# Optimization experiments

Measured on AMD Instinct MI355X. Metric: run time of the kernel, lower is better.

The kernel has to match this reference:

```python
import jax, jax.numpy as jnp
import numpy as np

EMBED_DIM = 1024
ATTN_DIM = 1024
BATCH = 4
SEQ = 2048


def setup_inputs() -> dict:
    key = jax.random.key(0)
    k1, k2, k3, k4 = jax.random.split(key, 4)
    embedded = jax.random.normal(k1, (BATCH, SEQ, EMBED_DIM), dtype=jnp.float32)
    # torch Linear weights have shape [out_features, in_features]
    scale = 1.0 / np.sqrt(EMBED_DIM)
    W_K = jax.random.uniform(k2, (ATTN_DIM, EMBED_DIM), dtype=jnp.float32, minval=-scale, maxval=scale)
    W_Q = jax.random.uniform(k3, (ATTN_DIM, EMBED_DIM), dtype=jnp.float32, minval=-scale, maxval=scale)
    W_V = jax.random.uniform(k4, (ATTN_DIM, EMBED_DIM), dtype=jnp.float32, minval=-scale, maxval=scale)
    return {"embedded": embedded, "W_K": W_K, "W_Q": W_Q, "W_V": W_V}


def reference(embedded, W_K, W_Q, W_V):
    # embedded: [B, L, E]; W_*: [A, E] (torch Linear layout, applied as x @ W.T)
    L = embedded.shape[1]
    A = W_K.shape[0]
    K = jnp.einsum('ble,ae->bla', embedded, W_K)
    Q = jnp.einsum('ble,ae->bla', embedded, W_Q)
    V = jnp.einsum('ble,ae->bla', embedded, W_V)
    att = jnp.einsum('bqa,bka->bqk', Q, K) / jnp.sqrt(jnp.float32(A))  # [B, L, L]
    causal = jnp.tril(jnp.ones((L, L), dtype=bool))  # lower-triangular mask
    att = jnp.where(causal, att, -jnp.inf)
    att = jax.nn.softmax(att, axis=-1)
    return jnp.einsum('bqk,bka->bqa', att, V)
```

## Files before the change

### kernel.cpp

```cpp
#include <hip/hip_runtime.h>
#include <hip/hip_bf16.h>
#include <stdint.h>

#define BATCH 4
#define SEQ   2048
#define EMB   1024
#define ADIM  1024

typedef __attribute__((ext_vector_type(8))) short  short8;
typedef __attribute__((ext_vector_type(4))) float  float4v;

static __device__ __forceinline__ unsigned short f2bf(float f) {
    unsigned int u = __float_as_uint(f);
    u += 0x7FFFu + ((u >> 16) & 1u);
    return (unsigned short)(u >> 16);
}

static __device__ __forceinline__ uint2 pack4(float4v v) {
    uint2 r;
    r.x = (unsigned)f2bf(v.x) | ((unsigned)f2bf(v.y) << 16);
    r.y = (unsigned)f2bf(v.z) | ((unsigned)f2bf(v.w) << 16);
    return r;
}

static __device__ __forceinline__ void gload16(const void* g, void* l) {
    __builtin_amdgcn_global_load_lds(
        (const __attribute__((address_space(1))) void*)g,
        (__attribute__((address_space(3))) void*)l, 16, 0, 0);
}

__global__ __launch_bounds__(256) void zero_kernel(float* __restrict__ p)
{
    const int i = (blockIdx.x * 256 + threadIdx.x) * 4;
    *(float4v*)(p + i) = float4v{0.f, 0.f, 0.f, 0.f};
}

__global__ __launch_bounds__(256) void cvt_all_kernel(
    const float* __restrict__ X,  const float* __restrict__ Wk,
    const float* __restrict__ Wq, const float* __restrict__ Wv,
    unsigned short* __restrict__ Xb,  unsigned short* __restrict__ Wkb,
    unsigned short* __restrict__ Wqb, unsigned short* __restrict__ Wvb)
{
    const int bI = blockIdx.x;
    const float* src; unsigned short* dst; int off;
    if (bI < 4096)      { src = X;  dst = Xb;  off = bI; }
    else if (bI < 4608) { src = Wk; dst = Wkb; off = bI - 4096; }
    else if (bI < 5120) { src = Wq; dst = Wqb; off = bI - 4608; }
    else                { src = Wv; dst = Wvb; off = bI - 5120; }
    const int i = (off * 256 + threadIdx.x) * 8;
    float4v a = *(const float4v*)(src + i);
    float4v b = *(const float4v*)(src + i + 4);
    uint2 pa = pack4(a), pb = pack4(b);
    uint4 o; o.x = pa.x; o.y = pa.y; o.z = pb.x; o.w = pb.y;
    *(uint4*)(dst + i) = o;
}

static __device__ __forceinline__ void gemm_core(
    const unsigned short* __restrict__ A, const unsigned short* __restrict__ B,
    int lda, int ldb, int m0, int n0, int kend,
    unsigned short* As, unsigned short* Bs, float4v acc[4][4])
{
    const int tid  = threadIdx.x;
    const int r    = tid >> 2;
    const int c8   = (tid & 3) << 3;
    const int lane = tid & 63;
    const int wave = tid >> 6;
    const int quad = lane >> 4;
    const int l16  = lane & 15;
    const int wm   = (wave >> 1) << 6;
    const int wn   = (wave & 1) << 6;

    const unsigned short* Ag = A + (size_t)(m0 + r) * lda + c8;
    const unsigned short* Bg = B + (size_t)(n0 + r) * ldb + c8;
    unsigned short* Al = As + tid * 8;
    unsigned short* Bl = Bs + tid * 8;
    const int niter = kend >> 5;

    #define ISSUE(k0, st) do { \
        unsigned short* al_ = Al + (st) * 4096; \
        unsigned short* bl_ = Bl + (st) * 4096; \
        gload16(Ag + (k0),                        al_); \
        gload16(Ag + (k0) + (size_t)64 * lda,     al_ + 2048); \
        gload16(Bg + (k0),                        bl_); \
        gload16(Bg + (k0) + (size_t)64 * ldb,     bl_ + 2048); \
    } while (0)

    ISSUE(0, 0);
    ISSUE(32, 1);

    int ci = 0;
    int ii = 2;
    for (int it = 0; it < niter; ++it) {
        const int knext = (it + 2 < niter) ? ((it + 2) << 5) : 0;
        ISSUE(knext, ii);
        asm volatile("s_waitcnt vmcnt(8)" ::: "memory");
        asm volatile("s_barrier" ::: "memory");

        const unsigned short* Ah = As + ci * 4096;
        const unsigned short* Bh = Bs + ci * 4096;
        short8 af[4], bfr[4];
        #pragma unroll
        for (int i = 0; i < 4; ++i)
            af[i] = *(const short8*)&Ah[(wm + 16 * i + l16) * 32 + quad * 8];
        #pragma unroll
        for (int j = 0; j < 4; ++j)
            bfr[j] = *(const short8*)&Bh[(wn + 16 * j + l16) * 32 + quad * 8];
        #pragma unroll
        for (int i = 0; i < 4; ++i)
            #pragma unroll
            for (int j = 0; j < 4; ++j)
                acc[i][j] = __builtin_amdgcn_mfma_f32_16x16x32_bf16(af[i], bfr[j], acc[i][j], 0, 0, 0);

        asm volatile("s_barrier" ::: "memory");
        ci = (ci == 2) ? 0 : ci + 1;
        ii = (ii == 2) ? 0 : ii + 1;
    }
    asm volatile("s_waitcnt vmcnt(0)" ::: "memory");
    #undef ISSUE
}

#define DECL_TILE_IDX() \
    const int lane = threadIdx.x & 63; \
    const int wave = threadIdx.x >> 6; \
    const int quad = lane >> 4; \
    const int l16  = lane & 15; \
    const int wm   = (wave >> 1) << 6; \
    const int wn   = (wave & 1) << 6;

__global__ __launch_bounds__(256, 3) void qkv_kernel(
    const unsigned short* __restrict__ Xb, const unsigned short* __restrict__ Wqb,
    const unsigned short* __restrict__ Wkb, const unsigned short* __restrict__ Wvb,
    unsigned short* __restrict__ Qb, unsigned short* __restrict__ Kb,
    unsigned short* __restrict__ Vtb)
{
    __shared__ __align__(16) unsigned short As[3 * 128 * 32];
    __shared__ __align__(16) unsigned short Bs[3 * 128 * 32];
    const int idx   = blockIdx.x;
    const int mlow  = idx & 7;
    const int n0    = ((idx >> 3) & 7) << 7;
    const int rest  = idx >> 6;
    const int mhigh = rest & 7;
    const int z     = rest >> 3;
    const int m0    = ((mhigh << 3) | mlow) << 7;
    const unsigned short* W = (z == 0) ? Wqb : (z == 1) ? Wkb : Wvb;

    float4v acc[4][4];
    #pragma unroll
    for (int i = 0; i < 4; ++i)
        #pragma unroll
        for (int j = 0; j < 4; ++j)
            acc[i][j] = float4v{0.f, 0.f, 0.f, 0.f};

    gemm_core(Xb, W, EMB, EMB, m0, n0, EMB, As, Bs, acc);

    DECL_TILE_IDX();
    #pragma unroll
    for (int i = 0; i < 4; ++i)
        #pragma unroll
        for (int j = 0; j < 4; ++j)
            #pragma unroll
            for (int rr = 0; rr < 4; ++rr) {
                const int row = m0 + wm + 16 * i + quad * 4 + rr;
                const int col = n0 + wn + 16 * j + l16;
                const unsigned short v = f2bf(acc[i][j][rr]);
                if (z == 0)      Qb[(size_t)row * ADIM + col] = v;
                else if (z == 1) Kb[(size_t)row * ADIM + col] = v;
                else {
                    const int bb = row >> 11;
                    const int l  = row & (SEQ - 1);
                    Vtb[((size_t)(bb * ADIM + col) << 11) + l] = v;
                }
            }
}

__global__ __launch_bounds__(256, 3) void s_kernel(
    const unsigned short* __restrict__ Qb, const unsigned short* __restrict__ Kb,
    unsigned short* __restrict__ E, float* __restrict__ rowsum)
{
    const int idx = blockIdx.x;
    const int b   = idx & 3;
    const int tri = idx >> 2;
    int qt = 0;
    while (((qt + 1) * (qt + 2)) / 2 <= tri) ++qt;
    const int kt = tri - (qt * (qt + 1)) / 2;
    const int q0 = qt << 7;
    const int k0 = kt << 7;

    __shared__ __align__(16) unsigned short As[3 * 128 * 32];
    __shared__ __align__(16) unsigned short Bs[3 * 128 * 32];

    float4v acc[4][4];
    #pragma unroll
    for (int i = 0; i < 4; ++i)
        #pragma unroll
        for (int j = 0; j < 4; ++j)
            acc[i][j] = float4v{0.f, 0.f, 0.f, 0.f};

    gemm_core(Qb + (size_t)b * SEQ * ADIM, Kb + (size_t)b * SEQ * ADIM,
              ADIM, ADIM, q0, k0, ADIM, As, Bs, acc);

    unsigned short* Eb = E + (size_t)b * SEQ * SEQ;
    float* rsb = rowsum + (size_t)b * SEQ;
    DECL_TILE_IDX();
    const float scale = 0.03125f;
    #pragma unroll
    for (int i = 0; i < 4; ++i)
        #pragma unroll
        for (int rr = 0; rr < 4; ++rr) {
            const int row = q0 + wm + 16 * i + quad * 4 + rr;
            float s = 0.f;
            #pragma unroll
            for (int j = 0; j < 4; ++j) {
                const int col = k0 + wn + 16 * j + l16;
                float e = (col <= row) ? __expf(acc[i][j][rr] * scale) : 0.f;
                s += e;
                Eb[(size_t)row * SEQ + col] = f2bf(e);
            }
            s += __shfl_xor(s, 1);
            s += __shfl_xor(s, 2);
            s += __shfl_xor(s, 4);
            s += __shfl_xor(s, 8);
            if (l16 == 0) atomicAdd(&rsb[row], s);
        }
}

__global__ __launch_bounds__(256, 3) void pv_kernel(
    const unsigned short* __restrict__ E, const unsigned short* __restrict__ Vtb,
    const float* __restrict__ rowsum, float* __restrict__ out)
{
    const int idx = blockIdx.x;
    const int t   = 15 - (idx >> 5);
    const int rem = idx & 31;
    const int b   = rem >> 3;
    const int a0  = (rem & 7) << 7;
    const int q0  = t << 7;

    __shared__ __align__(16) unsigned short As[3 * 128 * 32];
    __shared__ __align__(16) unsigned short Bs[3 * 128 * 32];

    float4v acc[4][4];
    #pragma unroll
    for (int i = 0; i < 4; ++i)
        #pragma unroll
        for (int j = 0; j < 4; ++j)
            acc[i][j] = float4v{0.f, 0.f, 0.f, 0.f};

    gemm_core(E + (size_t)b * SEQ * SEQ, Vtb + (size_t)b * ADIM * SEQ,
              SEQ, SEQ, q0, a0, q0 + 128, As, Bs, acc);

    float* ob = out + (size_t)b * SEQ * ADIM;
    const float* rsb = rowsum + (size_t)b * SEQ;
    DECL_TILE_IDX();
    #pragma unroll
    for (int i = 0; i < 4; ++i)
        #pragma unroll
        for (int rr = 0; rr < 4; ++rr) {
            const int row = q0 + wm + 16 * i + quad * 4 + rr;
            const float inv = 1.0f / rsb[row];
            #pragma unroll
            for (int j = 0; j < 4; ++j) {
                const int col = a0 + wn + 16 * j + l16;
                ob[(size_t)row * ADIM + col] = acc[i][j][rr] * inv;
            }
        }
}

extern "C" void kernel_launch(void* const* d_in, const int* in_sizes, int n_in,
                              void* d_out, int out_size, void* d_ws, size_t ws_size,
                              hipStream_t stream)
{
    const float* X  = (const float*)d_in[0];
    const float* Wk = (const float*)d_in[1];
    const float* Wq = (const float*)d_in[2];
    const float* Wv = (const float*)d_in[3];
    float* out = (float*)d_out;

    const size_t MB = 1024 * 1024;
    char* ws = (char*)d_ws;
    unsigned short* Xb  = (unsigned short*)(ws);
    unsigned short* Wqb = (unsigned short*)(ws + 16 * MB);
    unsigned short* Wkb = (unsigned short*)(ws + 18 * MB);
    unsigned short* Wvb = (unsigned short*)(ws + 20 * MB);
    unsigned short* E   = (unsigned short*)(ws);
    unsigned short* Qb  = (unsigned short*)(ws + 64 * MB);
    unsigned short* Kb  = (unsigned short*)(ws + 80 * MB);
    unsigned short* Vtb = (unsigned short*)(ws + 96 * MB);
    float*          rowsum = (float*)(ws + 112 * MB);

    hipLaunchKernelGGL(zero_kernel, dim3(BATCH * SEQ / 1024), dim3(256), 0, stream, rowsum);
    hipLaunchKernelGGL(cvt_all_kernel, dim3(5632), dim3(256), 0, stream,
                       X, Wk, Wq, Wv, Xb, Wkb, Wqb, Wvb);
    hipLaunchKernelGGL(qkv_kernel, dim3(1536), dim3(256), 0, stream,
                       Xb, Wqb, Wkb, Wvb, Qb, Kb, Vtb);
    hipLaunchKernelGGL(s_kernel, dim3(4 * 136), dim3(256), 0, stream, Qb, Kb, E, rowsum);
    hipLaunchKernelGGL(pv_kernel, dim3(512), dim3(256), 0, stream, E, Vtb, rowsum, out);
}
```

Before: 252.0 us.

## Fold W_Q and W_K into a single matrix to drop the K projection

Precomputes M = W_Q^T W_K (scaled) as a weight-only GEMM, then forms Q' = X·M and uses X directly as keys in the score GEMM, so the separate K projection GEMM is removed. A transposing bf16 conversion kernel is added for W_Q and W_K, and the rowsum zeroing is merged into the conversion kernel, cutting one launch. The cost is an extra small 1024x1024x1024 GEMM, and precision shifts because M is rounded to bf16 before it is applied.

Result: no change. 256.8 us (+1.9%).

```diff
diff --git a/kernel.cpp b/kernel.cpp
--- a/kernel.cpp
+++ b/kernel.cpp
@@ -29,30 +29,57 @@
         (__attribute__((address_space(3))) void*)l, 16, 0, 0);
 }
 
-__global__ __launch_bounds__(256) void zero_kernel(float* __restrict__ p)
-{
-    const int i = (blockIdx.x * 256 + threadIdx.x) * 4;
-    *(float4v*)(p + i) = float4v{0.f, 0.f, 0.f, 0.f};
-}
-
 __global__ __launch_bounds__(256) void cvt_all_kernel(
-    const float* __restrict__ X,  const float* __restrict__ Wk,
-    const float* __restrict__ Wq, const float* __restrict__ Wv,
-    unsigned short* __restrict__ Xb,  unsigned short* __restrict__ Wkb,
-    unsigned short* __restrict__ Wqb, unsigned short* __restrict__ Wvb)
+    const float* __restrict__ X,  const float* __restrict__ Wv,
+    unsigned short* __restrict__ Xb, unsigned short* __restrict__ Wvb,
+    float* __restrict__ rowsum)
 {
     const int bI = blockIdx.x;
+    if (bI >= 4608) {
+        const int i = ((bI - 4608) * 256 + threadIdx.x) * 4;
+        *(float4v*)(rowsum + i) = float4v{0.f, 0.f, 0.f, 0.f};
+        return;
+    }
     const float* src; unsigned short* dst; int off;
-    if (bI < 4096)      { src = X;  dst = Xb;  off = bI; }
-    else if (bI < 4608) { src = Wk; dst = Wkb; off = bI - 4096; }
-    else if (bI < 5120) { src = Wq; dst = Wqb; off = bI - 4608; }
-    else                { src = Wv; dst = Wvb; off = bI - 5120; }
+    if (bI < 4096) { src = X;  dst = Xb;  off = bI; }
+    else           { src = Wv; dst = Wvb; off = bI - 4096; }
     const int i = (off * 256 + threadIdx.x) * 8;
     float4v a = *(const float4v*)(src + i);
     float4v b = *(const float4v*)(src + i + 4);
     uint2 pa = pack4(a), pb = pack4(b);
     uint4 o; o.x = pa.x; o.y = pa.y; o.z = pb.x; o.w = pb.y;
     *(uint4*)(dst + i) = o;
+}
+
+__global__ __launch_bounds__(256) void tcvt_kernel(
+    const float* __restrict__ Wq, const float* __restrict__ Wk,
+    unsigned short* __restrict__ WqT, unsigned short* __restrict__ WkT)
+{
+    __shared__ unsigned short T[64][72];
+    const int z    = blockIdx.x >> 8;
+    const int tile = blockIdx.x & 255;
+    const int ti = tile >> 4;
+    const int tj = tile & 15;
+    const float* W = z ? Wk : Wq;
+    unsigned short* WT = z ? WkT : WqT;
+    const int t  = threadIdx.x;
+    const int r  = t >> 2;
+    const int c  = (t & 3) << 4;
+
+    const float* src = W + (size_t)(ti * 64 + r) * EMB + tj * 64 + c;
+    #pragma unroll
+    for (int u = 0; u < 4; ++u) {
+        float4v v = *(const float4v*)(src + 4 * u);
+        uint2 p = pack4(v);
+        *(uint2*)&T[r][c + 4 * u] = p;
+    }
+    __syncthreads();
+    unsigned short tmp[16];
+    #pragma unroll
+    for (int u = 0; u < 16; ++u) tmp[u] = T[c + u][r];
+    unsigned short* dst = WT + (size_t)(tj * 64 + r) * EMB + ti * 64 + c;
+    *(uint4*)(dst)     = *(uint4*)&tmp[0];
+    *(uint4*)(dst + 8) = *(uint4*)&tmp[8];
 }
 
 static __device__ __forceinline__ void gemm_core(
@@ -79,17 +106,16 @@
     #define ISSUE(k0, st) do { \
         unsigned short* al_ = Al + (st) * 4096; \
         unsigned short* bl_ = Bl + (st) * 4096; \
-        gload16(Ag + (k0),                        al_); \
-        gload16(Ag + (k0) + (size_t)64 * lda,     al_ + 2048); \
-        gload16(Bg + (k0),                        bl_); \
-        gload16(Bg + (k0) + (size_t)64 * ldb,     bl_ + 2048); \
+        gload16(Ag + (k0),                    al_); \
+        gload16(Ag + (k0) + (size_t)64 * lda, al_ + 2048); \
+        gload16(Bg + (k0),                    bl_); \
+        gload16(Bg + (k0) + (size_t)64 * ldb, bl_ + 2048); \
     } while (0)
 
     ISSUE(0, 0);
     ISSUE(32, 1);
 
-    int ci = 0;
-    int ii = 2;
+    int ci = 0, ii = 2;
     for (int it = 0; it < niter; ++it) {
         const int knext = (it + 2 < niter) ? ((it + 2) << 5) : 0;
         ISSUE(knext, ii);
@@ -127,22 +153,52 @@
     const int wm   = (wave >> 1) << 6; \
     const int wn   = (wave & 1) << 6;
 
-__global__ __launch_bounds__(256, 3) void qkv_kernel(
-    const unsigned short* __restrict__ Xb, const unsigned short* __restrict__ Wqb,
-    const unsigned short* __restrict__ Wkb, const unsigned short* __restrict__ Wvb,
-    unsigned short* __restrict__ Qb, unsigned short* __restrict__ Kb,
-    unsigned short* __restrict__ Vtb)
+__global__ __launch_bounds__(256, 3) void m_kernel(
+    const unsigned short* __restrict__ WkT, const unsigned short* __restrict__ WqT,
+    unsigned short* __restrict__ Mt)
+{
+    __shared__ __align__(16) unsigned short As[3 * 128 * 32];
+    __shared__ __align__(16) unsigned short Bs[3 * 128 * 32];
+    const int m0 = (blockIdx.x >> 3) << 7;
+    const int n0 = (blockIdx.x & 7) << 7;
+
+    float4v acc[4][4];
+    #pragma unroll
+    for (int i = 0; i < 4; ++i)
+        #pragma unroll
+        for (int j = 0; j < 4; ++j)
+            acc[i][j] = float4v{0.f, 0.f, 0.f, 0.f};
+
+    gemm_core(WkT, WqT, EMB, EMB, m0, n0, EMB, As, Bs, acc);
+
+    DECL_TILE_IDX();
+    const float scale = 0.03125f;
+    #pragma unroll
+    for (int i = 0; i < 4; ++i)
+        #pragma unroll
+        for (int j = 0; j < 4; ++j)
+            #pragma unroll
+            for (int rr = 0; rr < 4; ++rr) {
+                const int row = m0 + wm + 16 * i + quad * 4 + rr;
+                const int col = n0 + wn + 16 * j + l16;
+                Mt[(size_t)row * EMB + col] = f2bf(acc[i][j][rr] * scale);
+            }
+}
+
+__global__ __launch_bounds__(256, 3) void qv_kernel(
+    const unsigned short* __restrict__ Xb, const unsigned short* __restrict__ Mt,
+    const unsigned short* __restrict__ Wvb,
+    unsigned short* __restrict__ Qpb, unsigned short* __restrict__ Vtb)
 {
     __shared__ __align__(16) unsigned short As[3 * 128 * 32];
     __shared__ __align__(16) unsigned short Bs[3 * 128 * 32];
     const int idx   = blockIdx.x;
     const int mlow  = idx & 7;
     const int n0    = ((idx >> 3) & 7) << 7;
-    const int rest  = idx >> 6;
-    const int mhigh = rest & 7;
-    const int z     = rest >> 3;
+    const int mhigh = (idx >> 6) & 7;
+    const int z     = idx >> 9;
     const int m0    = ((mhigh << 3) | mlow) << 7;
-    const unsigned short* W = (z == 0) ? Wqb : (z == 1) ? Wkb : Wvb;
+    const unsigned short* W = (z == 0) ? Mt : Wvb;
 
     float4v acc[4][4];
     #pragma unroll
@@ -163,8 +219,7 @@
                 const int row = m0 + wm + 16 * i + quad * 4 + rr;
                 const int col = n0 + wn + 16 * j + l16;
                 const unsigned short v = f2bf(acc[i][j][rr]);
-                if (z == 0)      Qb[(size_t)row * ADIM + col] = v;
-                else if (z == 1) Kb[(size_t)row * ADIM + col] = v;
+                if (z == 0) Qpb[(size_t)row * ADIM + col] = v;
                 else {
                     const int bb = row >> 11;
                     const int l  = row & (SEQ - 1);
@@ -174,7 +229,7 @@
 }
 
 __global__ __launch_bounds__(256, 3) void s_kernel(
-    const unsigned short* __restrict__ Qb, const unsigned short* __restrict__ Kb,
+    const unsigned short* __restrict__ Qpb, const unsigned short* __restrict__ Xb,
     unsigned short* __restrict__ E, float* __restrict__ rowsum)
 {
     const int idx = blockIdx.x;
@@ -196,13 +251,12 @@
         for (int j = 0; j < 4; ++j)
             acc[i][j] = float4v{0.f, 0.f, 0.f, 0.f};
 
-    gemm_core(Qb + (size_t)b * SEQ * ADIM, Kb + (size_t)b * SEQ * ADIM,
-              ADIM, ADIM, q0, k0, ADIM, As, Bs, acc);
+    gemm_core(Qpb + (size_t)b * SEQ * ADIM, Xb + (size_t)b * SEQ * EMB,
+              ADIM, EMB, q0, k0, EMB, As, Bs, acc);
 
     unsigned short* Eb = E + (size_t)b * SEQ * SEQ;
     float* rsb = rowsum + (size_t)b * SEQ;
     DECL_TILE_IDX();
-    const float scale = 0.03125f;
     #pragma unroll
     for (int i = 0; i < 4; ++i)
         #pragma unroll
@@ -212,7 +266,7 @@
             #pragma unroll
             for (int j = 0; j < 4; ++j) {
                 const int col = k0 + wn + 16 * j + l16;
-                float e = (col <= row) ? __expf(acc[i][j][rr] * scale) : 0.f;
+                float e = (col <= row) ? __expf(acc[i][j][rr]) : 0.f;
                 s += e;
                 Eb[(size_t)row * SEQ + col] = f2bf(e);
             }
@@ -278,20 +332,22 @@
     const size_t MB = 1024 * 1024;
     char* ws = (char*)d_ws;
     unsigned short* Xb  = (unsigned short*)(ws);
-    unsigned short* Wqb = (unsigned short*)(ws + 16 * MB);
-    unsigned short* Wkb = (unsigned short*)(ws + 18 * MB);
-    unsigned short* Wvb = (unsigned short*)(ws + 20 * MB);
-    unsigned short* E   = (unsigned short*)(ws);
-    unsigned short* Qb  = (unsigned short*)(ws + 64 * MB);
-    unsigned short* Kb  = (unsigned short*)(ws + 80 * MB);
-    unsigned short* Vtb = (unsigned short*)(ws + 96 * MB);
-    float*          rowsum = (float*)(ws + 112 * MB);
-
-    hipLaunchKernelGGL(zero_kernel, dim3(BATCH * SEQ / 1024), dim3(256), 0, stream, rowsum);
-    hipLaunchKernelGGL(cvt_all_kernel, dim3(5632), dim3(256), 0, stream,
-                       X, Wk, Wq, Wv, Xb, Wkb, Wqb, Wvb);
-    hipLaunchKernelGGL(qkv_kernel, dim3(1536), dim3(256), 0, stream,
-                       Xb, Wqb, Wkb, Wvb, Qb, Kb, Vtb);
-    hipLaunchKernelGGL(s_kernel, dim3(4 * 136), dim3(256), 0, stream, Qb, Kb, E, rowsum);
+    unsigned short* Wvb = (unsigned short*)(ws + 16 * MB);
+    unsigned short* WqT = (unsigned short*)(ws + 18 * MB);
+    unsigned short* WkT = (unsigned short*)(ws + 20 * MB);
+    unsigned short* Mt  = (unsigned short*)(ws + 22 * MB);
+    unsigned short* Qpb = (unsigned short*)(ws + 24 * MB);
+    unsigned short* E   = (unsigned short*)(ws + 40 * MB);
+    unsigned short* Vtb = (unsigned short*)(ws + 72 * MB);
+    float*          rowsum = (float*)(ws + 88 * MB);
+
+    hipLaunchKernelGGL(cvt_all_kernel, dim3(4616), dim3(256), 0, stream,
+                       X, Wv, Xb, Wvb, rowsum);
+    hipLaunchKernelGGL(tcvt_kernel, dim3(512), dim3(256), 0, stream,
+                       Wq, Wk, WqT, WkT);
+    hipLaunchKernelGGL(m_kernel, dim3(64), dim3(256), 0, stream, WkT, WqT, Mt);
+    hipLaunchKernelGGL(qv_kernel, dim3(1024), dim3(256), 0, stream,
+                       Xb, Mt, Wvb, Qpb, Vtb);
+    hipLaunchKernelGGL(s_kernel, dim3(4 * 136), dim3(256), 0, stream, Qpb, Xb, E, rowsum);
     hipLaunchKernelGGL(pv_kernel, dim3(512), dim3(256), 0, stream, E, Vtb, rowsum, out);
 }
```
